# Optimization experiments

Hardware: AMD Instinct MI355X
Metric: run time of the kernel (lower is better)

## Reference

```python
import jax, jax.numpy as jnp
import numpy as np

N_CHANNELS = 1024
N_HEADS = 16
SEQ = 2048
BATCH = 2


def setup_inputs() -> dict:
    key = jax.random.key(0)
    k1, k2, k3 = jax.random.split(key, 3)
    x = jax.random.normal(k1, (BATCH, SEQ, N_CHANNELS), dtype=jnp.float32)
    qkv_w = jax.random.normal(k2, (3 * N_CHANNELS, N_CHANNELS), dtype=jnp.float32) * 0.02
    qkv_b = jnp.zeros((3 * N_CHANNELS,), dtype=jnp.float32)
    proj_w = jax.random.normal(k3, (N_CHANNELS, N_CHANNELS), dtype=jnp.float32) * 0.02
    proj_b = jnp.zeros((N_CHANNELS,), dtype=jnp.float32)
    return {"x": x, "qkv_w": qkv_w, "qkv_b": qkv_b, "proj_w": proj_w, "proj_b": proj_b}


def reference(x, qkv_w, qkv_b, proj_w, proj_b):
    bs, t, c = x.shape
    h = N_HEADS
    hd = c // h
    scale = hd ** (-0.5)
    # qkv projection: torch Linear is x @ W^T + b
    qkv = x @ qkv_w.T + qkv_b  # [B, T, 3C]
    qkv = qkv.reshape(bs, t, 3, h, hd)
    q, k, v = qkv[:, :, 0], qkv[:, :, 1], qkv[:, :, 2]  # each [B, T, H, hd]
    logits = jnp.einsum('bthc,bshc->bhts', q, k) * scale  # [B, H, T, T]
    # causal mask: log(tril(ones)) -> 0 below diag, -inf above
    causal = jnp.tril(jnp.ones((t, t), dtype=bool))
    logits = jnp.where(causal[None, None], logits, -jnp.inf)
    attn = jax.nn.softmax(logits, axis=-1)
    out = jnp.einsum('bhts,bshc->bthc', attn, v).reshape(bs, t, c)
    out = out @ proj_w.T + proj_b
    return out
```

## Files before the change

### kernel.cpp

```cpp
#include <hip/hip_runtime.h>

typedef __bf16 bf16x8 __attribute__((ext_vector_type(8)));
typedef float f32x4 __attribute__((ext_vector_type(4)));

__device__ inline ushort f2bf(float f) {
    unsigned u = __builtin_bit_cast(unsigned, f);
    unsigned r = (u + 0x7FFFu + ((u >> 16) & 1u)) >> 16;
    return (ushort)r;
}
__device__ inline uint4 pack8(const float* f) {
    uint4 r;
    r.x = (unsigned)f2bf(f[0]) | ((unsigned)f2bf(f[1]) << 16);
    r.y = (unsigned)f2bf(f[2]) | ((unsigned)f2bf(f[3]) << 16);
    r.z = (unsigned)f2bf(f[4]) | ((unsigned)f2bf(f[5]) << 16);
    r.w = (unsigned)f2bf(f[6]) | ((unsigned)f2bf(f[7]) << 16);
    return r;
}

#define MFMA_BF16(a, b, c) __builtin_amdgcn_mfma_f32_16x16x32_bf16(a, b, c, 0, 0, 0)
#define GLDS(g, l) __builtin_amdgcn_global_load_lds( \
    (const __attribute__((address_space(1))) void*)(g), \
    (__attribute__((address_space(3))) void*)(l), 16, 0, 0)

#define QSCALE 0.18033688011112042f

__global__ __launch_bounds__(256) void convert3(
    const float* __restrict__ s0, ushort* __restrict__ d0,
    const float* __restrict__ s1, ushort* __restrict__ d1,
    const float* __restrict__ s2, ushort* __restrict__ d2)
{
    const int i = blockIdx.x * 256 + threadIdx.x;
    const float* s; ushort* d; int off;
    if (i < 524288)      { s = s0; d = d0; off = i; }
    else if (i < 917504) { s = s1; d = d1; off = i - 524288; }
    else                 { s = s2; d = d2; off = i - 917504; }
    const float4* f = (const float4*)s + off * 2;
    float fa[8];
    *(float4*)&fa[0] = f[0];
    *(float4*)&fa[4] = f[1];
    ((uint4*)d)[off] = pack8(fa);
}

__global__ __launch_bounds__(256) void gemm_qkv(
    const ushort* __restrict__ A, const ushort* __restrict__ B,
    const float* __restrict__ bias,
    ushort* __restrict__ outQ, ushort* __restrict__ outK, ushort* __restrict__ outV,
    int N, int K)
{
    __shared__ __align__(16) ushort SMEM[17408];
    ushort* As = SMEM;
    ushort* Bs = SMEM + 8192;

    const int tid = threadIdx.x;
    const int w = tid >> 6;
    const int lane = tid & 63;
    const int l15 = lane & 15;
    const int quad = lane >> 4;
    const int m0 = blockIdx.x * 128;
    const int n0 = blockIdx.y * 128;
    const int wr = (w & 1) * 64;
    const int wc = (w >> 1) * 64;

    f32x4 acc[4][4] = {};

    for (int k0 = 0; k0 < K; k0 += 64) {
        __syncthreads();
#pragma unroll
        for (int j = 0; j < 4; j++) {
            const int r0 = w * 32 + j * 8;
            const int row = r0 + (lane >> 3);
            const int gcol = ((lane & 7) ^ (row & 7)) * 8;
            GLDS(A + (size_t)(m0 + row) * K + k0 + gcol, As + r0 * 64);
            GLDS(B + (size_t)(n0 + row) * K + k0 + gcol, Bs + r0 * 64);
        }
        __syncthreads();

        bf16x8 af[4][2], bf[4][2];
#pragma unroll
        for (int i = 0; i < 4; i++)
#pragma unroll
            for (int kk = 0; kk < 2; kk++) {
                const int ra = wr + i * 16 + l15;
                const int rb = wc + i * 16 + l15;
                const int ua = ((kk * 4 + quad) ^ (ra & 7)) * 8;
                const int ub = ((kk * 4 + quad) ^ (rb & 7)) * 8;
                af[i][kk] = *(const bf16x8*)&As[ra * 64 + ua];
                bf[i][kk] = *(const bf16x8*)&Bs[rb * 64 + ub];
            }
#pragma unroll
        for (int kk = 0; kk < 2; kk++)
#pragma unroll
            for (int mi = 0; mi < 4; mi++)
#pragma unroll
                for (int ni = 0; ni < 4; ni++)
                    acc[mi][ni] = MFMA_BF16(af[mi][kk], bf[ni][kk], acc[mi][ni]);
    }

    const int which = n0 >> 10;
    ushort* Ct = SMEM;
    __syncthreads();
    if (which == 2) {
#pragma unroll
        for (int mi = 0; mi < 4; mi++)
#pragma unroll
            for (int ni = 0; ni < 4; ni++)
#pragma unroll
                for (int r = 0; r < 4; r++) {
                    const int m_loc = wr + mi * 16 + quad * 4 + r;
                    const int n_loc = wc + ni * 16 + l15;
                    Ct[n_loc * 136 + m_loc] =
                        f2bf(acc[mi][ni][r] + bias[n0 + n_loc]);
                }
        __syncthreads();
        const int b = m0 >> 11;
#pragma unroll
        for (int i = 0; i < 8; i++) {
            const int vi = tid + i * 256;
            const int n_loc = vi >> 4, mblk = vi & 15;
            const uint4 val = *(const uint4*)&Ct[n_loc * 136 + mblk * 8];
            const int t = (m0 & 2047) + mblk * 8;
            const int c = (n0 + n_loc) & 1023;
            const int h = c >> 6, d = c & 63;
            *(uint4*)&outV[((size_t)(b * 16 + h) * 64 + d) * 2048 + t] = val;
        }
    } else {
        const float qs = (which == 0) ? QSCALE : 1.0f;
#pragma unroll
        for (int mi = 0; mi < 4; mi++)
#pragma unroll
            for (int ni = 0; ni < 4; ni++)
#pragma unroll
                for (int r = 0; r < 4; r++) {
                    const int m_loc = wr + mi * 16 + quad * 4 + r;
                    const int n_loc = wc + ni * 16 + l15;
                    Ct[m_loc * 136 + n_loc] =
                        f2bf((acc[mi][ni][r] + bias[n0 + n_loc]) * qs);
                }
        __syncthreads();
        ushort* outP = (which == 0) ? outQ : outK;
        const int hb = (n0 & 1023) >> 6;
        const int b = m0 >> 11;
#pragma unroll
        for (int i = 0; i < 8; i++) {
            const int vi = tid + i * 256;
            const int m_loc = vi >> 4, u = vi & 15;
            const uint4 val = *(const uint4*)&Ct[m_loc * 136 + u * 8];
            const int t = (m0 & 2047) + m_loc;
            const int h = hb + (u >> 3);
            const int d8 = (u & 7) * 8;
            *(uint4*)&outP[((size_t)(b * 16 + h)) * 131072 + (size_t)t * 64 + d8] = val;
        }
    }
}

__global__ __launch_bounds__(256) void gemm_proj(
    const ushort* __restrict__ A, const ushort* __restrict__ B,
    const float* __restrict__ bias, float* __restrict__ outD)
{
    const int N = 1024, K = 1024;
    __shared__ __align__(16) ushort SMEM[12288];
    ushort* As = SMEM;
    ushort* Bs = SMEM + 4096;

    const int tid = threadIdx.x;
    const int w = tid >> 6;
    const int lane = tid & 63;
    const int l15 = lane & 15;
    const int quad = lane >> 4;
    const int m0 = blockIdx.x * 64;
    const int n0 = blockIdx.y * 128;
    const int wr = (w & 1) * 32;
    const int wc = (w >> 1) * 64;

    f32x4 acc[2][4] = {};

    for (int k0 = 0; k0 < K; k0 += 64) {
        __syncthreads();
#pragma unroll
        for (int j = 0; j < 2; j++) {
            const int r0 = w * 16 + j * 8;
            const int row = r0 + (lane >> 3);
            const int gcol = ((lane & 7) ^ (row & 7)) * 8;
            GLDS(A + (size_t)(m0 + row) * K + k0 + gcol, As + r0 * 64);
        }
#pragma unroll
        for (int j = 0; j < 4; j++) {
            const int r0 = w * 32 + j * 8;
            const int row = r0 + (lane >> 3);
            const int gcol = ((lane & 7) ^ (row & 7)) * 8;
            GLDS(B + (size_t)(n0 + row) * K + k0 + gcol, Bs + r0 * 64);
        }
        __syncthreads();

        bf16x8 af[2][2], bf[4][2];
#pragma unroll
        for (int kk = 0; kk < 2; kk++) {
#pragma unroll
            for (int mi = 0; mi < 2; mi++) {
                const int ra = wr + mi * 16 + l15;
                af[mi][kk] = *(const bf16x8*)&As[ra * 64 + (((kk * 4 + quad) ^ (ra & 7)) * 8)];
            }
#pragma unroll
            for (int ni = 0; ni < 4; ni++) {
                const int rb = wc + ni * 16 + l15;
                bf[ni][kk] = *(const bf16x8*)&Bs[rb * 64 + (((kk * 4 + quad) ^ (rb & 7)) * 8)];
            }
        }
#pragma unroll
        for (int kk = 0; kk < 2; kk++)
#pragma unroll
            for (int mi = 0; mi < 2; mi++)
#pragma unroll
                for (int ni = 0; ni < 4; ni++)
                    acc[mi][ni] = MFMA_BF16(af[mi][kk], bf[ni][kk], acc[mi][ni]);
    }

    float* Cf = (float*)SMEM;
#pragma unroll
    for (int cch = 0; cch < 2; cch++) {
        __syncthreads();
        if ((wc >> 6) == cch) {
#pragma unroll
            for (int mi = 0; mi < 2; mi++)
#pragma unroll
                for (int ni = 0; ni < 4; ni++)
#pragma unroll
                    for (int r = 0; r < 4; r++) {
                        const int m_loc = wr + mi * 16 + quad * 4 + r;
                        const int nl = ni * 16 + l15;
                        Cf[m_loc * 68 + nl] = acc[mi][ni][r] + bias[n0 + cch * 64 + nl];
                    }
        }
        __syncthreads();
#pragma unroll
        for (int i = 0; i < 4; i++) {
            const int vi = tid + i * 256;
            const int m_loc = vi >> 4, u = vi & 15;
            const float4 val = *(const float4*)&Cf[m_loc * 68 + u * 4];
            *(float4*)&outD[(size_t)(m0 + m_loc) * N + n0 + cch * 64 + u * 4] = val;
        }
    }
}

__global__ __launch_bounds__(256) void attn3(
    const ushort* __restrict__ Q, const ushort* __restrict__ K,
    const ushort* __restrict__ Vt, ushort* __restrict__ O)
{
    __shared__ __align__(16) ushort KV[2][2][64 * 64];
    __shared__ __align__(16) __bf16 Ps[4][32 * 72];

    const int bh = blockIdx.x;
    const int qt = 15 - blockIdx.y;
    const int q0 = qt * 128;
    const int tid = threadIdx.x;
    const int w = tid >> 6;
    const int lane = tid & 63;
    const int l15 = lane & 15;
    const int quad = lane >> 4;

    auto stage = [&](int kt, int b) {
        const int t0 = kt * 64;
#pragma unroll
        for (int j = 0; j < 2; j++) {
            const int r0 = w * 16 + j * 8;
            const int row = r0 + (lane >> 3);
            const int gcol = ((lane & 7) ^ (row & 7)) * 8;
            GLDS(K + ((size_t)bh * 2048 + t0 + row) * 64 + gcol, &KV[b][0][r0 * 64]);
            GLDS(Vt + ((size_t)bh * 64 + row) * 2048 + t0 + gcol, &KV[b][1][r0 * 64]);
        }
    };

    bf16x8 qf[2][2];
#pragma unroll
    for (int mi = 0; mi < 2; mi++) {
        const ushort* qb = Q + ((size_t)bh * 2048 + q0 + w * 32 + mi * 16 + l15) * 64;
        qf[mi][0] = *(const bf16x8*)(qb + quad * 8);
        qf[mi][1] = *(const bf16x8*)(qb + 32 + quad * 8);
    }

    bf16x8 ones;
#pragma unroll
    for (int j = 0; j < 8; j++) ones[j] = (__bf16)1.0f;

    f32x4 oacc[2][4] = {};
    f32x4 lacc[2] = {};

    stage(0, 0);
    const int ktmax = 2 * qt + 1;

    for (int kt = 0; kt <= ktmax; kt++) {
        __syncthreads();
        if (kt < ktmax) stage(kt + 1, (kt + 1) & 1);

        const ushort* Ks = &KV[kt & 1][0][0];
        const ushort* Vs = &KV[kt & 1][1][0];
        const int t0 = kt * 64;

        f32x4 sacc[2][4] = {};
#pragma unroll
        for (int cb = 0; cb < 4; cb++) {
            const int rr = cb * 16 + l15;
            bf16x8 b0 = *(const bf16x8*)&Ks[rr * 64 + ((quad ^ (rr & 7)) * 8)];
            bf16x8 b1 = *(const bf16x8*)&Ks[rr * 64 + (((4 + quad) ^ (rr & 7)) * 8)];
#pragma unroll
            for (int mi = 0; mi < 2; mi++) {
                sacc[mi][cb] = MFMA_BF16(qf[mi][0], b0, sacc[mi][cb]);
                sacc[mi][cb] = MFMA_BF16(qf[mi][1], b1, sacc[mi][cb]);
            }
        }

        __bf16* pw = &Ps[w][0];
        __builtin_amdgcn_wave_barrier();
        if (t0 + 63 > q0 + w * 32) {
#pragma unroll
            for (int mi = 0; mi < 2; mi++)
#pragma unroll
                for (int cb = 0; cb < 4; cb++)
#pragma unroll
                    for (int r = 0; r < 4; r++) {
                        const int col = t0 + cb * 16 + l15;
                        const int row = q0 + w * 32 + mi * 16 + quad * 4 + r;
                        const float x = (col > row) ? -1e30f : sacc[mi][cb][r];
                        pw[(mi * 16 + quad * 4 + r) * 72 + cb * 16 + l15] =
                            (__bf16)__builtin_exp2f(x);
                    }
        } else {
#pragma unroll
            for (int mi = 0; mi < 2; mi++)
#pragma unroll
                for (int cb = 0; cb < 4; cb++)
#pragma unroll
                    for (int r = 0; r < 4; r++)
                        pw[(mi * 16 + quad * 4 + r) * 72 + cb * 16 + l15] =
                            (__bf16)__builtin_exp2f(sacc[mi][cb][r]);
        }
        __builtin_amdgcn_s_waitcnt(0xC07F);
        __builtin_amdgcn_wave_barrier();

#pragma unroll
        for (int kc = 0; kc < 2; kc++) {
            bf16x8 afr[2];
#pragma unroll
            for (int mi = 0; mi < 2; mi++)
                afr[mi] = *(const bf16x8*)&pw[(mi * 16 + l15) * 72 + kc * 32 + quad * 8];
#pragma unroll
            for (int cb = 0; cb < 4; cb++) {
                const int rr = cb * 16 + l15;
                bf16x8 bfr = *(const bf16x8*)&Vs[rr * 64 + (((kc * 4 + quad) ^ (rr & 7)) * 8)];
#pragma unroll
                for (int mi = 0; mi < 2; mi++)
                    oacc[mi][cb] = MFMA_BF16(afr[mi], bfr, oacc[mi][cb]);
            }
#pragma unroll
            for (int mi = 0; mi < 2; mi++)
                lacc[mi] = MFMA_BF16(afr[mi], ones, lacc[mi]);
        }
    }

    const int b = bh >> 4, h = bh & 15;
#pragma unroll
    for (int mi = 0; mi < 2; mi++)
#pragma unroll
        for (int r = 0; r < 4; r++) {
            const float inv = 1.0f / lacc[mi][r];
            const int row = q0 + w * 32 + mi * 16 + quad * 4 + r;
#pragma unroll
            for (int cb = 0; cb < 4; cb++) {
                const int col = h * 64 + cb * 16 + l15;
                O[((size_t)b * 2048 + row) * 1024 + col] = f2bf(oacc[mi][cb][r] * inv);
            }
        }
}

extern "C" void kernel_launch(void* const* d_in, const int* in_sizes, int n_in,
                              void* d_out, int out_size, void* d_ws, size_t ws_size,
                              hipStream_t stream) {
    const float* x      = (const float*)d_in[0];
    const float* qkv_w  = (const float*)d_in[1];
    const float* qkv_b  = (const float*)d_in[2];
    const float* proj_w = (const float*)d_in[3];
    const float* proj_b = (const float*)d_in[4];

    ushort* XbOb  = (ushort*)d_ws + 16;
    ushort* Wqkv  = XbOb + 4194304;
    ushort* Wproj = Wqkv + 3145728;
    ushort* Qb    = Wproj + 1048576;
    ushort* Kb    = Qb + 4194304;
    ushort* Vt    = Kb + 4194304;

    convert3<<<4096, 256, 0, stream>>>(x, XbOb, qkv_w, Wqkv, proj_w, Wproj);
    gemm_qkv<<<dim3(32, 24), 256, 0, stream>>>(XbOb, Wqkv, qkv_b,
                                               Qb, Kb, Vt, 3072, 1024);
    attn3<<<dim3(32, 16), 256, 0, stream>>>(Qb, Kb, Vt, XbOb);
    gemm_proj<<<dim3(64, 8), 256, 0, stream>>>(XbOb, Wproj, proj_b, (float*)d_out);
}
```

Measured before the change: 209.8 us.

## Split long causal attention rows across two blocks with separate combine kernel

Attention now uses 64-row query tiles. The 24 longest tiles have their key range split into two chunks processed by separate blocks, which write bf16 partial outputs and row sums to workspace. A new combine kernel adds the partials and normalizes them. The goal is better load balance and more blocks (1792 instead of 512) for the causal triangle. The cost is an extra launch, partial-result traffic, and bf16 rounding of the unnormalized partials.

Result: faster. 198.7 us (-5.3%).

```diff
diff --git a/kernel.cpp b/kernel.cpp
--- a/kernel.cpp
+++ b/kernel.cpp
@@ -7,6 +7,10 @@
     unsigned u = __builtin_bit_cast(unsigned, f);
     unsigned r = (u + 0x7FFFu + ((u >> 16) & 1u)) >> 16;
     return (ushort)r;
+}
+__device__ inline float bf2f(ushort u) {
+    unsigned x = ((unsigned)u) << 16;
+    return __builtin_bit_cast(float, x);
 }
 __device__ inline uint4 pack8(const float* f) {
     uint4 r;
@@ -82,10 +86,8 @@
             for (int kk = 0; kk < 2; kk++) {
                 const int ra = wr + i * 16 + l15;
                 const int rb = wc + i * 16 + l15;
-                const int ua = ((kk * 4 + quad) ^ (ra & 7)) * 8;
-                const int ub = ((kk * 4 + quad) ^ (rb & 7)) * 8;
-                af[i][kk] = *(const bf16x8*)&As[ra * 64 + ua];
-                bf[i][kk] = *(const bf16x8*)&Bs[rb * 64 + ub];
+                af[i][kk] = *(const bf16x8*)&As[ra * 64 + (((kk * 4 + quad) ^ (ra & 7)) * 8)];
+                bf[i][kk] = *(const bf16x8*)&Bs[rb * 64 + (((kk * 4 + quad) ^ (rb & 7)) * 8)];
             }
 #pragma unroll
         for (int kk = 0; kk < 2; kk++)
@@ -242,16 +244,25 @@
     }
 }
 
-__global__ __launch_bounds__(256) void attn3(
+__global__ __launch_bounds__(256) void attn_split(
     const ushort* __restrict__ Q, const ushort* __restrict__ K,
-    const ushort* __restrict__ Vt, ushort* __restrict__ O)
+    const ushort* __restrict__ Vt, ushort* __restrict__ O,
+    ushort* __restrict__ Opart, float* __restrict__ Lpart)
 {
     __shared__ __align__(16) ushort KV[2][2][64 * 64];
-    __shared__ __align__(16) __bf16 Ps[4][32 * 72];
+    __shared__ __align__(16) __bf16 Ps[4][16 * 64];
 
     const int bh = blockIdx.x;
-    const int qt = 15 - blockIdx.y;
-    const int q0 = qt * 128;
+    const int y = blockIdx.y;
+    int qt, k0, k1, chunk, split;
+    if (y < 48) {
+        qt = 31 - (y >> 1); chunk = y & 1; split = 1;
+        const int n = qt + 1, h = (n + 1) >> 1;
+        k0 = chunk ? h : 0; k1 = chunk ? n : h;
+    } else {
+        qt = 55 - y; chunk = 0; split = 0; k0 = 0; k1 = qt + 1;
+    }
+    const int q0 = qt * 64;
     const int tid = threadIdx.x;
     const int w = tid >> 6;
     const int lane = tid & 63;
@@ -270,106 +281,140 @@
         }
     };
 
-    bf16x8 qf[2][2];
-#pragma unroll
-    for (int mi = 0; mi < 2; mi++) {
-        const ushort* qb = Q + ((size_t)bh * 2048 + q0 + w * 32 + mi * 16 + l15) * 64;
-        qf[mi][0] = *(const bf16x8*)(qb + quad * 8);
-        qf[mi][1] = *(const bf16x8*)(qb + 32 + quad * 8);
-    }
+    const ushort* qbase = Q + ((size_t)bh * 2048 + q0 + w * 16 + l15) * 64;
+    bf16x8 qf0 = *(const bf16x8*)(qbase + quad * 8);
+    bf16x8 qf1 = *(const bf16x8*)(qbase + 32 + quad * 8);
 
     bf16x8 ones;
 #pragma unroll
     for (int j = 0; j < 8; j++) ones[j] = (__bf16)1.0f;
 
-    f32x4 oacc[2][4] = {};
-    f32x4 lacc[2] = {};
-
-    stage(0, 0);
-    const int ktmax = 2 * qt + 1;
-
-    for (int kt = 0; kt <= ktmax; kt++) {
-        __syncthreads();
-        if (kt < ktmax) stage(kt + 1, (kt + 1) & 1);
-
-        const ushort* Ks = &KV[kt & 1][0][0];
-        const ushort* Vs = &KV[kt & 1][1][0];
+    f32x4 oacc[4] = {};
+    f32x4 lacc = {};
+
+    stage(k0, 0);
+
+    for (int kt = k0; kt < k1; kt++) {
+        __syncthreads();
+        if (kt + 1 < k1) stage(kt + 1, (kt + 1 - k0) & 1);
+
+        const ushort* Ks = &KV[(kt - k0) & 1][0][0];
+        const ushort* Vs = &KV[(kt - k0) & 1][1][0];
         const int t0 = kt * 64;
 
-        f32x4 sacc[2][4] = {};
+        f32x4 sacc[4] = {};
 #pragma unroll
         for (int cb = 0; cb < 4; cb++) {
             const int rr = cb * 16 + l15;
             bf16x8 b0 = *(const bf16x8*)&Ks[rr * 64 + ((quad ^ (rr & 7)) * 8)];
             bf16x8 b1 = *(const bf16x8*)&Ks[rr * 64 + (((4 + quad) ^ (rr & 7)) * 8)];
-#pragma unroll
-            for (int mi = 0; mi < 2; mi++) {
-                sacc[mi][cb] = MFMA_BF16(qf[mi][0], b0, sacc[mi][cb]);
-                sacc[mi][cb] = MFMA_BF16(qf[mi][1], b1, sacc[mi][cb]);
-            }
+            sacc[cb] = MFMA_BF16(qf0, b0, sacc[cb]);
+            sacc[cb] = MFMA_BF16(qf1, b1, sacc[cb]);
         }
 
         __bf16* pw = &Ps[w][0];
         __builtin_amdgcn_wave_barrier();
-        if (t0 + 63 > q0 + w * 32) {
-#pragma unroll
-            for (int mi = 0; mi < 2; mi++)
-#pragma unroll
-                for (int cb = 0; cb < 4; cb++)
-#pragma unroll
-                    for (int r = 0; r < 4; r++) {
-                        const int col = t0 + cb * 16 + l15;
-                        const int row = q0 + w * 32 + mi * 16 + quad * 4 + r;
-                        const float x = (col > row) ? -1e30f : sacc[mi][cb][r];
-                        pw[(mi * 16 + quad * 4 + r) * 72 + cb * 16 + l15] =
-                            (__bf16)__builtin_exp2f(x);
-                    }
-        } else {
-#pragma unroll
-            for (int mi = 0; mi < 2; mi++)
-#pragma unroll
-                for (int cb = 0; cb < 4; cb++)
-#pragma unroll
-                    for (int r = 0; r < 4; r++)
-                        pw[(mi * 16 + quad * 4 + r) * 72 + cb * 16 + l15] =
-                            (__bf16)__builtin_exp2f(sacc[mi][cb][r]);
-        }
+#pragma unroll
+        for (int cb = 0; cb < 4; cb++)
+#pragma unroll
+            for (int r = 0; r < 4; r++) {
+                float x = sacc[cb][r];
+                if (kt == qt) {
+                    const int col = t0 + cb * 16 + l15;
+                    const int row = q0 + w * 16 + quad * 4 + r;
+                    if (col > row) x = -1e30f;
+                }
+                const int prow = quad * 4 + r;
+                const int unit = cb * 2 + (l15 >> 3);
+                pw[prow * 64 + ((unit ^ (prow & 7)) * 8) + (l15 & 7)] =
+                    (__bf16)__builtin_exp2f(x);
+            }
         __builtin_amdgcn_s_waitcnt(0xC07F);
         __builtin_amdgcn_wave_barrier();
 
 #pragma unroll
         for (int kc = 0; kc < 2; kc++) {
-            bf16x8 afr[2];
-#pragma unroll
-            for (int mi = 0; mi < 2; mi++)
-                afr[mi] = *(const bf16x8*)&pw[(mi * 16 + l15) * 72 + kc * 32 + quad * 8];
+            bf16x8 afr = *(const bf16x8*)&pw[l15 * 64 + (((kc * 4 + quad) ^ (l15 & 7)) * 8)];
 #pragma unroll
             for (int cb = 0; cb < 4; cb++) {
                 const int rr = cb * 16 + l15;
                 bf16x8 bfr = *(const bf16x8*)&Vs[rr * 64 + (((kc * 4 + quad) ^ (rr & 7)) * 8)];
-#pragma unroll
-                for (int mi = 0; mi < 2; mi++)
-                    oacc[mi][cb] = MFMA_BF16(afr[mi], bfr, oacc[mi][cb]);
-            }
-#pragma unroll
-            for (int mi = 0; mi < 2; mi++)
-                lacc[mi] = MFMA_BF16(afr[mi], ones, lacc[mi]);
-        }
-    }
-
-    const int b = bh >> 4, h = bh & 15;
-#pragma unroll
-    for (int mi = 0; mi < 2; mi++)
+                oacc[cb] = MFMA_BF16(afr, bfr, oacc[cb]);
+            }
+            lacc = MFMA_BF16(afr, ones, lacc);
+        }
+    }
+
+    if (!split) {
+        const int b = bh >> 4, h = bh & 15;
 #pragma unroll
         for (int r = 0; r < 4; r++) {
-            const float inv = 1.0f / lacc[mi][r];
-            const int row = q0 + w * 32 + mi * 16 + quad * 4 + r;
+            const float inv = 1.0f / lacc[r];
+            const int row = q0 + w * 16 + quad * 4 + r;
 #pragma unroll
             for (int cb = 0; cb < 4; cb++) {
                 const int col = h * 64 + cb * 16 + l15;
-                O[((size_t)b * 2048 + row) * 1024 + col] = f2bf(oacc[mi][cb][r] * inv);
-            }
-        }
+                O[((size_t)b * 2048 + row) * 1024 + col] = f2bf(oacc[cb][r] * inv);
+            }
+        }
+    } else {
+        const size_t slot2 = ((size_t)bh * 24 + (qt - 8)) * 2 + chunk;
+        if (l15 == 0) {
+#pragma unroll
+            for (int r = 0; r < 4; r++)
+                Lpart[slot2 * 64 + w * 16 + quad * 4 + r] = lacc[r];
+        }
+        __bf16* pw = &Ps[w][0];
+        __builtin_amdgcn_wave_barrier();
+#pragma unroll
+        for (int cb = 0; cb < 4; cb++)
+#pragma unroll
+            for (int r = 0; r < 4; r++) {
+                const int prow = quad * 4 + r;
+                const int unit = cb * 2 + (l15 >> 3);
+                pw[prow * 64 + ((unit ^ (prow & 7)) * 8) + (l15 & 7)] =
+                    (__bf16)oacc[cb][r];
+            }
+        __builtin_amdgcn_s_waitcnt(0xC07F);
+        __builtin_amdgcn_wave_barrier();
+        const int r = lane >> 2, u = lane & 3;
+        const int p0 = (2 * u) ^ (r & 7), p1 = (2 * u + 1) ^ (r & 7);
+        const uint4 a = *(const uint4*)&pw[r * 64 + p0 * 8];
+        const uint4 b = *(const uint4*)&pw[r * 64 + p1 * 8];
+        ushort* dst = Opart + slot2 * 4096 + (w * 16 + r) * 64 + u * 16;
+        *(uint4*)dst = a;
+        *(uint4*)(dst + 8) = b;
+    }
+}
+
+__global__ __launch_bounds__(256) void attn_combine(
+    const ushort* __restrict__ Opart, const float* __restrict__ Lpart,
+    ushort* __restrict__ O)
+{
+    const int bh = blockIdx.x;
+    const int qt = 8 + blockIdx.y;
+    const int tid = threadIdx.x;
+    const int row = tid >> 2;
+    const int cg = (tid & 3) * 16;
+    const size_t s = ((size_t)bh * 24 + (qt - 8)) * 2;
+    const ushort* p0 = Opart + s * 4096 + row * 64 + cg;
+    const ushort* p1 = p0 + 4096;
+    const float inv = 1.0f / (Lpart[s * 64 + row] + Lpart[(s + 1) * 64 + row]);
+    const int b = bh >> 4, h = bh & 15;
+    ushort* dst = O + ((size_t)b * 2048 + qt * 64 + row) * 1024 + h * 64 + cg;
+    ushort out[16];
+#pragma unroll
+    for (int v = 0; v < 2; v++) {
+        uint4 a = *(const uint4*)(p0 + v * 8);
+        uint4 c = *(const uint4*)(p1 + v * 8);
+        const ushort* ua = (const ushort*)&a;
+        const ushort* uc = (const ushort*)&c;
+#pragma unroll
+        for (int j = 0; j < 8; j++)
+            out[v * 8 + j] = f2bf((bf2f(ua[j]) + bf2f(uc[j])) * inv);
+    }
+    *(uint4*)dst = *(uint4*)&out[0];
+    *(uint4*)(dst + 8) = *(uint4*)&out[8];
 }
 
 extern "C" void kernel_launch(void* const* d_in, const int* in_sizes, int n_in,
@@ -387,10 +432,13 @@
     ushort* Qb    = Wproj + 1048576;
     ushort* Kb    = Qb + 4194304;
     ushort* Vt    = Kb + 4194304;
+    ushort* Opart = Vt + 4194304;
+    float*  Lpart = (float*)(Opart + 6291456);
 
     convert3<<<4096, 256, 0, stream>>>(x, XbOb, qkv_w, Wqkv, proj_w, Wproj);
     gemm_qkv<<<dim3(32, 24), 256, 0, stream>>>(XbOb, Wqkv, qkv_b,
                                                Qb, Kb, Vt, 3072, 1024);
-    attn3<<<dim3(32, 16), 256, 0, stream>>>(Qb, Kb, Vt, XbOb);
+    attn_split<<<dim3(32, 56), 256, 0, stream>>>(Qb, Kb, Vt, XbOb, Opart, Lpart);
+    attn_combine<<<dim3(32, 24), 256, 0, stream>>>(Opart, Lpart, XbOb);
     gemm_proj<<<dim3(64, 8), 256, 0, stream>>>(XbOb, Wproj, proj_b, (float*)d_out);
 }
```
